# Optimization experiments

Hardware: AMD Instinct MI355X
Metric: run time of the kernel (lower is better)

## Reference

```python
import jax, jax.numpy as jnp
import numpy as np

N, INPUTDIM, OUTDIM, GRIDSIZE = 32768, 64, 256, 32


def setup_inputs() -> dict:
    key = jax.random.key(0)
    k1, k2 = jax.random.split(key)
    x = jax.random.normal(k1, (N, INPUTDIM), dtype=jnp.float32)
    # xavier_uniform over tensor of shape (2, outdim, inputdim, gridsize):
    # fan_in = inputdim*gridsize, fan_out = outdim*gridsize (torch treats dim0=fan_out-ish,
    # but exact init scale is irrelevant for correctness; use a matching uniform range)
    fan_in = INPUTDIM * GRIDSIZE
    fan_out = OUTDIM * GRIDSIZE
    bound = float(np.sqrt(6.0 / (fan_in + fan_out)))
    fouriercoeffs = jax.random.uniform(
        k2, (2, OUTDIM, INPUTDIM, GRIDSIZE), dtype=jnp.float32,
        minval=-bound, maxval=bound)
    bias = jnp.zeros((1, OUTDIM), dtype=jnp.float32)
    return {"x": x, "fouriercoeffs": fouriercoeffs, "bias": bias}


def reference(x, fouriercoeffs, bias):
    # gridsize_param rounds back to GRIDSIZE at init -> static.
    g = fouriercoeffs.shape[-1]
    k = jnp.arange(1, g + 1, dtype=x.dtype)  # (g,)
    # Fourier feature expansion: (N, inputdim, g)
    xk = x[:, :, None] * k[None, None, :]
    c = jnp.cos(xk)
    s = jnp.sin(xk)
    # Contract over (inputdim, gridsize) -> two GEMMs over flattened dim
    y = jnp.einsum('nig,oig->no', c, fouriercoeffs[0])
    y = y + jnp.einsum('nig,oig->no', s, fouriercoeffs[1])
    y = y + bias  # (1, outdim) broadcasts over N
    return y
```

## Files before the change

### kernel.cpp

```cpp
#include <hip/hip_runtime.h>


#define IDIM 64
#define ODIM 256
#define KDIM 4096
#define BM 64

typedef __attribute__((ext_vector_type(8))) unsigned short ushort8_t;
typedef __bf16 bf16x8 __attribute__((ext_vector_type(8)));
typedef float floatx4 __attribute__((ext_vector_type(4)));

__device__ __forceinline__ unsigned short f2bf_rne(float f) {
  unsigned int u = __float_as_uint(f);
  return (unsigned short)((u + 0x7FFFu + ((u >> 16) & 1u)) >> 16);
}

__global__ void __launch_bounds__(256) wconv(const float* __restrict__ fc,
                                             unsigned short* __restrict__ Wr) {
  __shared__ unsigned short Sb[2][256][32];
  const int t = threadIdx.x;
  const int kt = blockIdx.x;

#pragma unroll
  for (int it = 0; it < 16; ++it) {
    int s = it * 256 + t;
    int r = s >> 3;
    int p = s & 7;
    int c = r >> 8;
    int o = r & 255;
    const float4 v =
        *(const float4*)(fc + ((size_t)c << 19) + o * 2048 + kt * 32 + p * 4);
    ushort4 w;
    w.x = f2bf_rne(v.x);
    w.y = f2bf_rne(v.y);
    w.z = f2bf_rne(v.z);
    w.w = f2bf_rne(v.w);
    *(ushort4*)&Sb[c][o][p * 4] = w;
  }
  __syncthreads();

#pragma unroll
  for (int it = 0; it < 8; ++it) {
    int gg = it * 256 + t;
    int lane = gg & 63;
    int j = (gg >> 6) & 7;
    int bb = gg >> 9;
    int wn2 = bb & 1;
    int wk = (bb >> 1) & 1;
    int o = wn2 * 128 + j * 16 + (lane & 15);
    int g0 = (lane >> 4) * 8;
    ushort8_t v = *(const ushort8_t*)&Sb[wk][o][g0];
    *(ushort8_t*)(Wr + ((size_t)kt * 2048 + gg) * 8) = v;
  }
}

__global__ void __launch_bounds__(256, 2) fkan_gemm(const float* __restrict__ X,
                                                    const unsigned short* __restrict__ Wr,
                                                    const float* __restrict__ bias,
                                                    float* __restrict__ out) {
  __shared__ __align__(16) unsigned char smem[66560];
  unsigned short* const AsBase = (unsigned short*)smem;
  float* const red = (float*)smem;

  const int t = threadIdx.x;
  const int wv = t >> 6;
  const int ln = t & 63;
  const int lm = ln & 15;
  const int quad = ln >> 4;
  const int wk = wv & 1;
  const int wn2 = wv >> 1;
  const int m0 = blockIdx.x * BM;

  const int arow = t >> 2;
  const int q = t & 3;
  const float g0f = (float)(8 * q + 1);

  const int ga_c = arow * 8 + (q ^ (arow & 7));
  const int ga_s = arow * 8 + ((4 + q) ^ (arow & 7));

  const unsigned short* const bwave = Wr + (size_t)(wk * 2 + wn2) * 4096 + ln * 8;

  floatx4 acc[4][8];
#pragma unroll
  for (int a = 0; a < 4; ++a)
#pragma unroll
    for (int b = 0; b < 8; ++b)
      acc[a][b] = (floatx4){0.0f, 0.0f, 0.0f, 0.0f};

  const float* xptr = X + (size_t)(m0 + arow) * IDIM;

  auto features = [&](float xv, int buf, int j) {
    const float inv2pi = 0.15915494309189535f;
    float u = xv * inv2pi;
    float u0 = u * g0f;
    float c1 = __builtin_amdgcn_cosf(u);
    float s1 = __builtin_amdgcn_sinf(u);
    float C = __builtin_amdgcn_cosf(u0);
    float S = __builtin_amdgcn_sinf(u0);
    bf16x8 cb, sb;
    cb[0] = (__bf16)C;
    sb[0] = (__bf16)S;
#pragma unroll
    for (int jj = 1; jj < 8; ++jj) {
      float Cn = __builtin_fmaf(C, c1, -(S * s1));
      float Sn = __builtin_fmaf(S, c1, (C * s1));
      C = Cn;
      S = Sn;
      cb[jj] = (__bf16)C;
      sb[jj] = (__bf16)S;
    }
    ushort8_t* As8 = (ushort8_t*)(AsBase + buf * 16384 + j * 4096);
    As8[ga_c] = __builtin_bit_cast(ushort8_t, cb);
    As8[ga_s] = __builtin_bit_cast(ushort8_t, sb);
  };

  bf16x8 breg[8];

  auto cluster = [&](int buf, int j, int reload_kt, bool do_reload) {
    const ushort8_t* A8 = (const ushort8_t*)(AsBase + buf * 16384 + j * 4096);
    const int ch = wk * 4 + quad;
    bf16x8 af[4];
#pragma unroll
    for (int mt = 0; mt < 4; ++mt) {
      int r = mt * 16 + lm;
      af[mt] = __builtin_bit_cast(bf16x8, A8[r * 8 + (ch ^ (r & 7))]);
    }
    const unsigned short* bn = bwave + (size_t)reload_kt * 16384;
    __builtin_amdgcn_s_setprio(1);
#pragma unroll
    for (int nt = 0; nt < 8; ++nt) {
#pragma unroll
      for (int mt = 0; mt < 4; ++mt)
        acc[mt][nt] = __builtin_amdgcn_mfma_f32_16x16x32_bf16(
            af[mt], breg[nt], acc[mt][nt], 0, 0, 0);
      if (do_reload)
        breg[nt] = __builtin_bit_cast(bf16x8, *(const ushort8_t*)(bn + nt * 512));
    }
    __builtin_amdgcn_s_setprio(0);
  };

  auto ktquad = [&](int s, int cur, int nxt) {
    int k0 = 4 * s;
    float xn0 = xptr[k0 + 4];
    float xn1 = xptr[k0 + 5];
    float xn2 = xptr[k0 + 6];
    float xn3 = xptr[k0 + 7];
    cluster(cur, 0, k0 + 1, true);
    features(xn0, nxt, 0);
    cluster(cur, 1, k0 + 2, true);
    features(xn1, nxt, 1);
    cluster(cur, 2, k0 + 3, true);
    features(xn2, nxt, 2);
    cluster(cur, 3, k0 + 4, true);
    features(xn3, nxt, 3);
    __syncthreads();
  };

#pragma unroll
  for (int nt = 0; nt < 8; ++nt)
    breg[nt] = __builtin_bit_cast(bf16x8, *(const ushort8_t*)(bwave + nt * 512));
  features(xptr[0], 0, 0);
  features(xptr[1], 0, 1);
  features(xptr[2], 0, 2);
  features(xptr[3], 0, 3);
  __syncthreads();

  for (int s = 0; s < 14; s += 2) {
    ktquad(s, 0, 1);
    ktquad(s + 1, 1, 0);
  }
  ktquad(14, 0, 1);

  cluster(1, 0, 61, true);
  cluster(1, 1, 62, true);
  cluster(1, 2, 63, true);
  cluster(1, 3, 0, false);

  __syncthreads();
  if (wk == 1) {
#pragma unroll
    for (int mt = 0; mt < 4; ++mt)
#pragma unroll
      for (int nt = 0; nt < 8; ++nt) {
        int col = wn2 * 128 + nt * 16 + lm;
#pragma unroll
        for (int idx = 0; idx < 4; ++idx)
          red[(mt * 16 + quad * 4 + idx) * 260 + col] = acc[mt][nt][idx];
      }
  }
  __syncthreads();
  if (wk == 0) {
#pragma unroll
    for (int nt = 0; nt < 8; ++nt) {
      int col = wn2 * 128 + nt * 16 + lm;
      float bv = bias[col];
#pragma unroll
      for (int mt = 0; mt < 4; ++mt) {
        int rbase = m0 + mt * 16 + quad * 4;
#pragma unroll
        for (int idx = 0; idx < 4; ++idx)
          out[(size_t)(rbase + idx) * ODIM + col] =
              acc[mt][nt][idx] + red[(mt * 16 + quad * 4 + idx) * 260 + col] + bv;
      }
    }
  }
}

extern "C" void kernel_launch(void* const* d_in, const int* in_sizes, int n_in,
                              void* d_out, int out_size, void* d_ws, size_t ws_size,
                              hipStream_t stream) {
  const float* x = (const float*)d_in[0];
  const float* fc = (const float*)d_in[1];
  const float* bias = (const float*)d_in[2];
  float* out = (float*)d_out;
  unsigned short* Wr = (unsigned short*)d_ws;

  hipLaunchKernelGGL(wconv, dim3(64), dim3(256), 0, stream, fc, Wr);
  hipLaunchKernelGGL(fkan_gemm, dim3(512), dim3(256), 0, stream, x, Wr, bias, out);
}
```

Before: 128.3 us.

## Split waves over output columns instead of K to drop cross-wave reduction

Each of the four waves now owns a 64-column slice of the output and walks the full K range (cos and sin chunks), rather than pairs of waves splitting K and reducing through shared memory. This removes the final LDS reduction, its two barriers and the larger shared buffer, and halves the accumulator registers. In exchange, each wave reads twice as many A fragments from LDS per step (8 instead of 4), which raises LDS traffic.

```diff
diff --git a/kernel.cpp b/kernel.cpp
--- a/kernel.cpp
+++ b/kernel.cpp
@@ -46,10 +46,10 @@
     int j = (gg >> 6) & 7;
     int bb = gg >> 9;
     int wn2 = bb & 1;
-    int wk = (bb >> 1) & 1;
+    int c = (bb >> 1) & 1;
     int o = wn2 * 128 + j * 16 + (lane & 15);
     int g0 = (lane >> 4) * 8;
-    ushort8_t v = *(const ushort8_t*)&Sb[wk][o][g0];
+    ushort8_t v = *(const ushort8_t*)&Sb[c][o][g0];
     *(ushort8_t*)(Wr + ((size_t)kt * 2048 + gg) * 8) = v;
   }
 }
@@ -58,17 +58,15 @@
                                                     const unsigned short* __restrict__ Wr,
                                                     const float* __restrict__ bias,
                                                     float* __restrict__ out) {
-  __shared__ __align__(16) unsigned char smem[66560];
-  unsigned short* const AsBase = (unsigned short*)smem;
-  float* const red = (float*)smem;
+  __shared__ __align__(16) unsigned short As[2][4][4096];
+  unsigned short* const AsBase = &As[0][0][0];
 
   const int t = threadIdx.x;
   const int wv = t >> 6;
   const int ln = t & 63;
   const int lm = ln & 15;
   const int quad = ln >> 4;
-  const int wk = wv & 1;
-  const int wn2 = wv >> 1;
+  const int wn = wv;
   const int m0 = blockIdx.x * BM;
 
   const int arow = t >> 2;
@@ -78,13 +76,15 @@
   const int ga_c = arow * 8 + (q ^ (arow & 7));
   const int ga_s = arow * 8 + ((4 + q) ^ (arow & 7));
 
-  const unsigned short* const bwave = Wr + (size_t)(wk * 2 + wn2) * 4096 + ln * 8;
-
-  floatx4 acc[4][8];
+  const int wn2 = wn >> 1;
+  const unsigned short* const bwave =
+      Wr + ((size_t)wn2 * 512 + (wn & 1) * 256 + ln) * 8;
+
+  floatx4 acc[4][4];
 #pragma unroll
   for (int a = 0; a < 4; ++a)
 #pragma unroll
-    for (int b = 0; b < 8; ++b)
+    for (int b = 0; b < 4; ++b)
       acc[a][b] = (floatx4){0.0f, 0.0f, 0.0f, 0.0f};
 
   const float* xptr = X + (size_t)(m0 + arow) * IDIM;
@@ -109,7 +109,7 @@
       cb[jj] = (__bf16)C;
       sb[jj] = (__bf16)S;
     }
-    ushort8_t* As8 = (ushort8_t*)(AsBase + buf * 16384 + j * 4096);
+    ushort8_t* As8 = (ushort8_t*)&As[buf][j][0];
     As8[ga_c] = __builtin_bit_cast(ushort8_t, cb);
     As8[ga_s] = __builtin_bit_cast(ushort8_t, sb);
   };
@@ -117,24 +117,30 @@
   bf16x8 breg[8];
 
   auto cluster = [&](int buf, int j, int reload_kt, bool do_reload) {
-    const ushort8_t* A8 = (const ushort8_t*)(AsBase + buf * 16384 + j * 4096);
-    const int ch = wk * 4 + quad;
-    bf16x8 af[4];
-#pragma unroll
-    for (int mt = 0; mt < 4; ++mt) {
-      int r = mt * 16 + lm;
-      af[mt] = __builtin_bit_cast(bf16x8, A8[r * 8 + (ch ^ (r & 7))]);
-    }
+    const ushort8_t* A8 = (const ushort8_t*)&As[buf][j][0];
+    bf16x8 af[8];
+#pragma unroll
+    for (int c = 0; c < 2; ++c)
+#pragma unroll
+      for (int mt = 0; mt < 4; ++mt) {
+        int r = mt * 16 + lm;
+        int ch = c * 4 + quad;
+        af[c * 4 + mt] =
+            __builtin_bit_cast(bf16x8, A8[r * 8 + (ch ^ (r & 7))]);
+      }
     const unsigned short* bn = bwave + (size_t)reload_kt * 16384;
     __builtin_amdgcn_s_setprio(1);
 #pragma unroll
-    for (int nt = 0; nt < 8; ++nt) {
+    for (int b = 0; b < 8; ++b) {
+      const int c = b >> 2;
+      const int nt = b & 3;
 #pragma unroll
       for (int mt = 0; mt < 4; ++mt)
         acc[mt][nt] = __builtin_amdgcn_mfma_f32_16x16x32_bf16(
-            af[mt], breg[nt], acc[mt][nt], 0, 0, 0);
+            af[c * 4 + mt], breg[b], acc[mt][nt], 0, 0, 0);
       if (do_reload)
-        breg[nt] = __builtin_bit_cast(bf16x8, *(const ushort8_t*)(bn + nt * 512));
+        breg[b] = __builtin_bit_cast(
+            bf16x8, *(const ushort8_t*)(bn + (c * 1024 + nt * 64) * 8));
     }
     __builtin_amdgcn_s_setprio(0);
   };
@@ -157,8 +163,10 @@
   };
 
 #pragma unroll
-  for (int nt = 0; nt < 8; ++nt)
-    breg[nt] = __builtin_bit_cast(bf16x8, *(const ushort8_t*)(bwave + nt * 512));
+  for (int b = 0; b < 8; ++b)
+    breg[b] = __builtin_bit_cast(
+        bf16x8,
+        *(const ushort8_t*)(bwave + ((b >> 2) * 1024 + (b & 3) * 64) * 8));
   features(xptr[0], 0, 0);
   features(xptr[1], 0, 1);
   features(xptr[2], 0, 2);
@@ -176,32 +184,16 @@
   cluster(1, 2, 63, true);
   cluster(1, 3, 0, false);
 
-  __syncthreads();
-  if (wk == 1) {
-#pragma unroll
-    for (int mt = 0; mt < 4; ++mt)
-#pragma unroll
-      for (int nt = 0; nt < 8; ++nt) {
-        int col = wn2 * 128 + nt * 16 + lm;
-#pragma unroll
-        for (int idx = 0; idx < 4; ++idx)
-          red[(mt * 16 + quad * 4 + idx) * 260 + col] = acc[mt][nt][idx];
-      }
-  }
-  __syncthreads();
-  if (wk == 0) {
-#pragma unroll
-    for (int nt = 0; nt < 8; ++nt) {
-      int col = wn2 * 128 + nt * 16 + lm;
-      float bv = bias[col];
-#pragma unroll
-      for (int mt = 0; mt < 4; ++mt) {
-        int rbase = m0 + mt * 16 + quad * 4;
-#pragma unroll
-        for (int idx = 0; idx < 4; ++idx)
-          out[(size_t)(rbase + idx) * ODIM + col] =
-              acc[mt][nt][idx] + red[(mt * 16 + quad * 4 + idx) * 260 + col] + bv;
-      }
+#pragma unroll
+  for (int nt = 0; nt < 4; ++nt) {
+    int col = wn * 64 + nt * 16 + lm;
+    float bv = bias[col];
+#pragma unroll
+    for (int mt = 0; mt < 4; ++mt) {
+      int rbase = m0 + mt * 16 + quad * 4;
+#pragma unroll
+      for (int idx = 0; idx < 4; ++idx)
+        out[(size_t)(rbase + idx) * ODIM + col] = acc[mt][nt][idx] + bv;
     }
   }
 }
```

Result: no change. 127.1 us (-1.0%).
